# Kernel optimization log

Hardware: AMD Instinct MI355X
Metric: run time of the kernel (lower is better)

## Reference

```python
import jax, jax.numpy as jnp
import numpy as np

B, T, D = 2, 2048, 1024
H, HD = 16, 64
MAX_LEN = 2048


def setup_inputs() -> dict:
    key = jax.random.key(0)
    ks = jax.random.split(key, 7)
    s = 0.02
    return {
        "x": jax.random.normal(ks[0], (B, T, D), dtype=jnp.float32),
        "qkv_w": jax.random.normal(ks[1], (3 * D, D), dtype=jnp.float32) * s,
        "qkv_b": jax.random.normal(ks[2], (3 * D,), dtype=jnp.float32) * s,
        "out_w": jax.random.normal(ks[3], (D, D), dtype=jnp.float32) * s,
        "out_b": jax.random.normal(ks[4], (D,), dtype=jnp.float32) * s,
        "rel_pos": jax.random.normal(ks[5], (2 * MAX_LEN - 1, HD), dtype=jnp.float32),
        "rpe_w": jax.random.normal(ks[6], (HD,), dtype=jnp.float32) * s,
    }


def reference(x, qkv_w, qkv_b, out_w, out_b, rel_pos, rpe_w):
    Bq, Tq, Dq = x.shape
    scale = HD ** -0.5
    qkv = x @ qkv_w.T + qkv_b  # [B,T,3D]
    qkv = qkv.reshape(Bq, Tq, 3, H, HD)
    q = qkv[:, :, 0].transpose(0, 2, 1, 3)  # [B,H,T,HD]
    k = qkv[:, :, 1].transpose(0, 2, 1, 3)
    v = qkv[:, :, 2].transpose(0, 2, 1, 3)
    scores = jnp.einsum('bhqd,bhkd->bhqk', q, k) * scale  # [B,H,T,T]
    # relative position bias: gather rel embeddings, project to scalar
    rel_idx = jnp.arange(Tq)[None, :] - jnp.arange(Tq)[:, None] + MAX_LEN - 1  # [T,T]
    bias = (rel_pos @ rpe_w)[rel_idx]  # project first (cheap), then gather -> [T,T]
    scores = scores + bias[None, None]
    attn = jax.nn.softmax(scores, axis=-1)
    out = jnp.einsum('bhqk,bhkd->bhqd', attn, v)  # [B,H,T,HD]
    out = out.transpose(0, 2, 1, 3).reshape(Bq, Tq, Dq)
    return out @ out_w.T + out_b
```

## Files before the change

kernel.cpp:

```cpp
#include <hip/hip_runtime.h>
#include <math.h>

#define B_ 2
#define T_ 2048
#define D_ 1024
#define H_ 16
#define HD_ 64
#define MAXLEN_ 2048
#define N3D_ 3072
#define M_ (B_ * T_)
#define KA 1024

#define SCALE_L2E 0.18033688011116215f
#define L2E 1.4426950408889634f

typedef unsigned short ushort_t;
typedef __attribute__((ext_vector_type(8))) short short8;
typedef __attribute__((ext_vector_type(4))) float floatx4;
#define MFMA16(a, b, c) __builtin_amdgcn_mfma_f32_16x16x32_bf16(a, b, c, 0, 0, 0)

static __device__ __forceinline__ ushort_t f2bf(float f) {
    unsigned u = __float_as_uint(f);
    unsigned r = (u + 0x7FFFu + ((u >> 16) & 1u)) >> 16;
    return (ushort_t)r;
}
static __device__ __forceinline__ unsigned pack2bf(float a, float b) {
    unsigned ua = __float_as_uint(a), ub = __float_as_uint(b);
    ua = ua + 0x7FFFu + ((ua >> 16) & 1u);
    ub = ub + 0x7FFFu + ((ub >> 16) & 1u);
    return (ua >> 16) | (ub & 0xFFFF0000u);
}

static __device__ __forceinline__ void gld16(const ushort_t* g, ushort_t* l) {
    __builtin_amdgcn_global_load_lds(
        (const __attribute__((address_space(1))) void*)g,
        (__attribute__((address_space(3))) void*)l, 16, 0, 0);
}

__global__ __launch_bounds__(256) void cvt_all(
    const float* __restrict__ x, const float* __restrict__ qw,
    const float* __restrict__ ow,
    ushort_t* __restrict__ Xc, ushort_t* __restrict__ QWc,
    ushort_t* __restrict__ OWc)
{
    const int row = blockIdx.x;
    const float* src; ushort_t* dst; int r;
    if (row < M_)            { src = x;  dst = Xc;  r = row; }
    else if (row < M_ + N3D_){ src = qw; dst = QWc; r = row - M_; }
    else                     { src = ow; dst = OWc; r = row - M_ - N3D_; }
    const int c = threadIdx.x * 4;
    float4 v = *(const float4*)(src + (size_t)r * 1024 + c);
    ushort4 hv;
    hv.x = f2bf(v.x); hv.y = f2bf(v.y); hv.z = f2bf(v.z); hv.w = f2bf(v.w);
    *(ushort4*)(dst + (size_t)r * KA + c) = hv;
}

__global__ __launch_bounds__(256) void qkv_mfma(
    const ushort_t* __restrict__ Ac, const ushort_t* __restrict__ Bc,
    const float* __restrict__ bias,
    ushort_t* __restrict__ Qs, ushort_t* __restrict__ Khi,
    ushort_t* __restrict__ Vt)
{
    __shared__ __align__(16) ushort_t As[16 * 512];
    __shared__ __align__(16) ushort_t Bs[16 * 512];
    const int tid = threadIdx.x;
    const int wv = tid >> 6, lane = tid & 63;
    const int l16 = lane & 15, quad = lane >> 4;
    const int wm = wv & 1, wn = wv >> 1;
    const int m0 = blockIdx.y * 128, n0 = blockIdx.x * 128;

    floatx4 acc[4][4];
#pragma unroll
    for (int i = 0; i < 4; ++i)
#pragma unroll
        for (int j = 0; j < 4; ++j) acc[i][j] = (floatx4){0.f, 0.f, 0.f, 0.f};

    for (int k0 = 0; k0 < KA; k0 += 64) {
        __syncthreads();
#pragma unroll
        for (int c = 0; c < 4; ++c) {
            const int b = wv * 4 + c;
            const int i = b >> 1, ks = b & 1;
            const int k = k0 + ks * 32 + quad * 8;
            gld16(Ac + (size_t)(m0 + i * 16 + l16) * KA + k, As + b * 512);
            gld16(Bc + (size_t)(n0 + i * 16 + l16) * KA + k, Bs + b * 512);
        }
        __syncthreads();
#pragma unroll
        for (int ks = 0; ks < 2; ++ks) {
            short8 af[4], bf[4];
#pragma unroll
            for (int ii = 0; ii < 4; ++ii)
                af[ii] = *(const short8*)(As + ((wm * 4 + ii) * 2 + ks) * 512 + lane * 8);
#pragma unroll
            for (int jj = 0; jj < 4; ++jj)
                bf[jj] = *(const short8*)(Bs + ((wn * 4 + jj) * 2 + ks) * 512 + lane * 8);
#pragma unroll
            for (int ii = 0; ii < 4; ++ii)
#pragma unroll
                for (int jj = 0; jj < 4; ++jj)
                    acc[ii][jj] = MFMA16(af[ii], bf[jj], acc[ii][jj]);
        }
    }

#pragma unroll
    for (int ii = 0; ii < 4; ++ii) {
#pragma unroll
        for (int r = 0; r < 4; ++r) {
            const int m = m0 + wm * 64 + ii * 16 + quad * 4 + r;
            const int bb = m >> 11, t = m & 2047;
#pragma unroll
            for (int jj = 0; jj < 4; ++jj) {
                const int n = n0 + wn * 64 + jj * 16 + l16;
                const int c = n >> 10, h = (n >> 6) & 15, hd = n & 63;
                const float v = acc[ii][jj][r] + bias[n];
                const size_t idx = (((size_t)bb * H_ + h) * T_ + t) * HD_ + hd;
                if (c == 0) { Qs[idx] = f2bf(v * SCALE_L2E); }
                else if (c == 1) { Khi[idx] = f2bf(v); }
                else { Vt[(((size_t)bb * H_ + h) * HD_ + hd) * T_ + t] = f2bf(v); }
            }
        }
    }
}

__global__ __launch_bounds__(256) void out_mfma(
    const ushort_t* __restrict__ Ac, const ushort_t* __restrict__ Bc,
    const float* __restrict__ bias, float* __restrict__ Out)
{
    __shared__ __align__(16) ushort_t As[16 * 512];
    __shared__ __align__(16) ushort_t Bs[8 * 512];
    const int tid = threadIdx.x;
    const int wv = tid >> 6, lane = tid & 63;
    const int l16 = lane & 15, quad = lane >> 4;
    const int wm = wv & 1, wn = wv >> 1;
    const int m0 = blockIdx.y * 128, n0 = blockIdx.x * 64;

    floatx4 acc[4][2];
#pragma unroll
    for (int i = 0; i < 4; ++i)
#pragma unroll
        for (int j = 0; j < 2; ++j) acc[i][j] = (floatx4){0.f, 0.f, 0.f, 0.f};

    for (int k0 = 0; k0 < KA; k0 += 64) {
        __syncthreads();
#pragma unroll
        for (int c = 0; c < 4; ++c) {
            const int b = wv * 4 + c;
            const int i = b >> 1, ks = b & 1;
            const int k = k0 + ks * 32 + quad * 8;
            gld16(Ac + (size_t)(m0 + i * 16 + l16) * KA + k, As + b * 512);
        }
#pragma unroll
        for (int c = 0; c < 2; ++c) {
            const int b = wv * 2 + c;
            const int j = b >> 1, ks = b & 1;
            const int k = k0 + ks * 32 + quad * 8;
            gld16(Bc + (size_t)(n0 + j * 16 + l16) * KA + k, Bs + b * 512);
        }
        __syncthreads();
#pragma unroll
        for (int ks = 0; ks < 2; ++ks) {
            short8 af[4], bf[2];
#pragma unroll
            for (int ii = 0; ii < 4; ++ii)
                af[ii] = *(const short8*)(As + ((wm * 4 + ii) * 2 + ks) * 512 + lane * 8);
#pragma unroll
            for (int jj = 0; jj < 2; ++jj)
                bf[jj] = *(const short8*)(Bs + ((wn * 2 + jj) * 2 + ks) * 512 + lane * 8);
#pragma unroll
            for (int ii = 0; ii < 4; ++ii)
#pragma unroll
                for (int jj = 0; jj < 2; ++jj)
                    acc[ii][jj] = MFMA16(af[ii], bf[jj], acc[ii][jj]);
        }
    }

#pragma unroll
    for (int ii = 0; ii < 4; ++ii) {
#pragma unroll
        for (int r = 0; r < 4; ++r) {
            const int m = m0 + wm * 64 + ii * 16 + quad * 4 + r;
#pragma unroll
            for (int jj = 0; jj < 2; ++jj) {
                const int n = n0 + wn * 32 + jj * 16 + l16;
                Out[(size_t)m * D_ + n] = acc[ii][jj][r] + bias[n];
            }
        }
    }
}

__global__ __launch_bounds__(64) void rpe_project(
    const float* __restrict__ rel_pos, const float* __restrict__ rpe_w,
    float* __restrict__ biasp)
{
    const int i = blockIdx.x;
    const int lane = threadIdx.x;
    float v = rel_pos[(size_t)i * HD_ + lane] * rpe_w[lane];
#pragma unroll
    for (int off = 32; off; off >>= 1) v += __shfl_down(v, off);
    if (lane == 0) biasp[i] = v * L2E;
}

__global__ __launch_bounds__(256) void attn_mfma(
    const ushort_t* __restrict__ Qs, const ushort_t* __restrict__ Khi,
    const ushort_t* __restrict__ Vt, const float* __restrict__ biasp,
    ushort_t* __restrict__ AOc)
{
    __shared__ __align__(16) ushort_t KS[8 * 512];
    __shared__ __align__(16) ushort_t VS[8 * 512];
    __shared__ __align__(16) ushort_t PS[4][2 * 512];

    const int i = blockIdx.x;
    const int bh = (i & 7) + 8 * (i >> 8);
    const int q0 = ((i >> 3) & 31) * 64;
    const int tid = threadIdx.x;
    const int wv = tid >> 6, lane = tid & 63;
    const int l16 = lane & 15, quad = lane >> 4;

    const int q = q0 + wv * 16 + l16;
    const size_t qoff = ((size_t)bh * T_ + q) * HD_ + quad * 8;
    const short8 qh0 = *(const short8*)(Qs + qoff);
    const short8 qh1 = *(const short8*)(Qs + qoff + 32);

    float l_r = 0.f;
    floatx4 o_acc[4];
#pragma unroll
    for (int g2 = 0; g2 < 4; ++g2) o_acc[g2] = (floatx4){0.f, 0.f, 0.f, 0.f};

    const ushort_t* gK = Khi + (size_t)bh * T_ * HD_;
    const ushort_t* gV = Vt + (size_t)bh * HD_ * T_;
    const int biasbase = 2047 + quad * 4 - q;

    const int qdbase = quad >> 1;
    ushort_t* pw = PS[wv];

    for (int k0 = 0; k0 < T_; k0 += 64) {
        __syncthreads();
        {
            const size_t krow = (size_t)(k0 + wv * 16 + l16) * HD_ + quad * 8;
            gld16(gK + krow,      KS + (wv * 2 + 0) * 512);
            gld16(gK + krow + 32, KS + (wv * 2 + 1) * 512);
            const size_t vrow = (size_t)(wv * 16 + l16) * T_ + k0 + quad * 8;
            gld16(gV + vrow,      VS + (wv * 2 + 0) * 512);
            gld16(gV + vrow + 32, VS + (wv * 2 + 1) * 512);
        }
        float4 bb[4];
#pragma unroll
        for (int g = 0; g < 4; ++g)
            __builtin_memcpy(&bb[g], biasp + (biasbase + k0 + g * 16), 16);
        __syncthreads();

#pragma unroll
        for (int g = 0; g < 4; ++g) {
            const short8 kh0 = *(const short8*)(KS + (g * 2 + 0) * 512 + lane * 8);
            const short8 kh1 = *(const short8*)(KS + (g * 2 + 1) * 512 + lane * 8);
            floatx4 a = (floatx4){0.f, 0.f, 0.f, 0.f};
            a = MFMA16(kh0, qh0, a);
            a = MFMA16(kh1, qh1, a);
            const float* bp = (const float*)&bb[g];
            float p0 = __builtin_amdgcn_exp2f(a[0] + bp[0]);
            float p1 = __builtin_amdgcn_exp2f(a[1] + bp[1]);
            float p2 = __builtin_amdgcn_exp2f(a[2] + bp[2]);
            float p3 = __builtin_amdgcn_exp2f(a[3] + bp[3]);
            l_r += (p0 + p1) + (p2 + p3);
            uint2 pkd;
            pkd.x = pack2bf(p0, p1);
            pkd.y = pack2bf(p2, p3);
            const int qd = 2 * (g & 1) + qdbase;
            *(uint2*)(pw + (g >> 1) * 512 + (qd * 16 + l16) * 8 + (quad & 1) * 4) = pkd;
        }
        const short8 p0 = *(const short8*)(pw + lane * 8);
        const short8 p1 = *(const short8*)(pw + 512 + lane * 8);

#pragma unroll
        for (int g2 = 0; g2 < 4; ++g2) {
            const short8 v0 = *(const short8*)(VS + (g2 * 2 + 0) * 512 + lane * 8);
            const short8 v1 = *(const short8*)(VS + (g2 * 2 + 1) * 512 + lane * 8);
            o_acc[g2] = MFMA16(v0, p0, o_acc[g2]);
            o_acc[g2] = MFMA16(v1, p1, o_acc[g2]);
        }
    }

    l_r += __shfl_xor(l_r, 16);
    l_r += __shfl_xor(l_r, 32);
    const float inv = 1.0f / l_r;
    const int bb2 = bh >> 4, h2 = bh & 15;
    const size_t m = (size_t)bb2 * T_ + q;
#pragma unroll
    for (int g2 = 0; g2 < 4; ++g2) {
        ushort4 hv;
        hv.x = f2bf(o_acc[g2][0] * inv);
        hv.y = f2bf(o_acc[g2][1] * inv);
        hv.z = f2bf(o_acc[g2][2] * inv);
        hv.w = f2bf(o_acc[g2][3] * inv);
        *(ushort4*)(AOc + m * KA + h2 * 64 + g2 * 16 + quad * 4) = hv;
    }
}

extern "C" void kernel_launch(void* const* d_in, const int* in_sizes, int n_in,
                              void* d_out, int out_size, void* d_ws, size_t ws_size,
                              hipStream_t stream)
{
    const float* x       = (const float*)d_in[0];
    const float* qkv_w   = (const float*)d_in[1];
    const float* qkv_b   = (const float*)d_in[2];
    const float* out_w   = (const float*)d_in[3];
    const float* out_b   = (const float*)d_in[4];
    const float* rel_pos = (const float*)d_in[5];
    const float* rpe_w   = (const float*)d_in[6];
    float* out = (float*)d_out;

    const size_t QE = (size_t)B_ * H_ * T_ * HD_;
    ushort_t* Qs  = (ushort_t*)d_ws;
    ushort_t* Khi = Qs  + QE;
    ushort_t* Vt  = Khi + QE;
    ushort_t* Xc  = Vt  + QE;
    ushort_t* QWc = Xc  + (size_t)M_ * KA;
    ushort_t* OWc = QWc + (size_t)N3D_ * KA;
    ushort_t* AOc = OWc + (size_t)D_ * KA;
    float* biasp  = (float*)(AOc + (size_t)M_ * KA);

    cvt_all<<<M_ + N3D_ + D_, 256, 0, stream>>>(x, qkv_w, out_w, Xc, QWc, OWc);
    rpe_project<<<2 * MAXLEN_ - 1, 64, 0, stream>>>(rel_pos, rpe_w, biasp);

    qkv_mfma<<<dim3(N3D_ / 128, M_ / 128), 256, 0, stream>>>(
        Xc, QWc, qkv_b, Qs, Khi, Vt);
    attn_mfma<<<1024, 256, 0, stream>>>(Qs, Khi, Vt, biasp, AOc);
    out_mfma<<<dim3(D_ / 64, M_ / 128), 256, 0, stream>>>(
        AOc, OWc, out_b, out);
}
```

Baseline: 282.9 us.

## Restructure attention kernel to 32x32 MFMA tiles with register-resident K/V

Rewrites the attention kernel around 32x32x16 bf16 MFMAs. Each wave owns a 32-key by 32-query score tile and a 32-head-dim slice of the output. K and V fragments are loaded straight from global memory into registers and prefetched one tile ahead, so the K/V LDS staging is gone. P is exchanged between waves through a double-buffered, XOR-swizzled LDS buffer with a single barrier per tile, and the row sums are combined across waves at the end. The P conversion now uses truncation instead of round-to-nearest bf16, which is slightly less accurate, and K/V reuse now relies on caches rather than shared memory.

Measured after the change: 377.2 us. 33.3% more time.

```diff
diff --git a/kernel.cpp b/kernel.cpp
--- a/kernel.cpp
+++ b/kernel.cpp
@@ -17,7 +17,9 @@
 typedef unsigned short ushort_t;
 typedef __attribute__((ext_vector_type(8))) short short8;
 typedef __attribute__((ext_vector_type(4))) float floatx4;
+typedef __attribute__((ext_vector_type(16))) float floatx16;
 #define MFMA16(a, b, c) __builtin_amdgcn_mfma_f32_16x16x32_bf16(a, b, c, 0, 0, 0)
+#define MFMA32(a, b, c) __builtin_amdgcn_mfma_f32_32x32x16_bf16(a, b, c, 0, 0, 0)
 
 static __device__ __forceinline__ ushort_t f2bf(float f) {
     unsigned u = __float_as_uint(f);
@@ -29,6 +31,9 @@
     ua = ua + 0x7FFFu + ((ua >> 16) & 1u);
     ub = ub + 0x7FFFu + ((ub >> 16) & 1u);
     return (ua >> 16) | (ub & 0xFFFF0000u);
+}
+static __device__ __forceinline__ unsigned packrtz(float a, float b) {
+    return __builtin_amdgcn_perm(__float_as_uint(b), __float_as_uint(a), 0x07060302u);
 }
 
 static __device__ __forceinline__ void gld16(const ushort_t* g, ushort_t* l) {
@@ -206,94 +211,95 @@
     const ushort_t* __restrict__ Vt, const float* __restrict__ biasp,
     ushort_t* __restrict__ AOc)
 {
-    __shared__ __align__(16) ushort_t KS[8 * 512];
-    __shared__ __align__(16) ushort_t VS[8 * 512];
-    __shared__ __align__(16) ushort_t PS[4][2 * 512];
+    __shared__ __align__(16) ushort_t PS[2][4096];
+    __shared__ float LS[2][64];
 
     const int i = blockIdx.x;
     const int bh = (i & 7) + 8 * (i >> 8);
     const int q0 = ((i >> 3) & 31) * 64;
     const int tid = threadIdx.x;
     const int wv = tid >> 6, lane = tid & 63;
-    const int l16 = lane & 15, quad = lane >> 4;
-
-    const int q = q0 + wv * 16 + l16;
-    const size_t qoff = ((size_t)bh * T_ + q) * HD_ + quad * 8;
-    const short8 qh0 = *(const short8*)(Qs + qoff);
-    const short8 qh1 = *(const short8*)(Qs + qoff + 32);
-
-    float l_r = 0.f;
-    floatx4 o_acc[4];
-#pragma unroll
-    for (int g2 = 0; g2 < 4; ++g2) o_acc[g2] = (floatx4){0.f, 0.f, 0.f, 0.f};
-
-    const ushort_t* gK = Khi + (size_t)bh * T_ * HD_;
-    const ushort_t* gV = Vt + (size_t)bh * HD_ * T_;
-    const int biasbase = 2047 + quad * 4 - q;
-
-    const int qdbase = quad >> 1;
-    ushort_t* pw = PS[wv];
-
-    for (int k0 = 0; k0 < T_; k0 += 64) {
-        __syncthreads();
-        {
-            const size_t krow = (size_t)(k0 + wv * 16 + l16) * HD_ + quad * 8;
-            gld16(gK + krow,      KS + (wv * 2 + 0) * 512);
-            gld16(gK + krow + 32, KS + (wv * 2 + 1) * 512);
-            const size_t vrow = (size_t)(wv * 16 + l16) * T_ + k0 + quad * 8;
-            gld16(gV + vrow,      VS + (wv * 2 + 0) * 512);
-            gld16(gV + vrow + 32, VS + (wv * 2 + 1) * 512);
-        }
-        float4 bb[4];
-#pragma unroll
-        for (int g = 0; g < 4; ++g)
-            __builtin_memcpy(&bb[g], biasp + (biasbase + k0 + g * 16), 16);
-        __syncthreads();
-
-#pragma unroll
-        for (int g = 0; g < 4; ++g) {
-            const short8 kh0 = *(const short8*)(KS + (g * 2 + 0) * 512 + lane * 8);
-            const short8 kh1 = *(const short8*)(KS + (g * 2 + 1) * 512 + lane * 8);
-            floatx4 a = (floatx4){0.f, 0.f, 0.f, 0.f};
-            a = MFMA16(kh0, qh0, a);
-            a = MFMA16(kh1, qh1, a);
-            const float* bp = (const float*)&bb[g];
-            float p0 = __builtin_amdgcn_exp2f(a[0] + bp[0]);
-            float p1 = __builtin_amdgcn_exp2f(a[1] + bp[1]);
-            float p2 = __builtin_amdgcn_exp2f(a[2] + bp[2]);
-            float p3 = __builtin_amdgcn_exp2f(a[3] + bp[3]);
-            l_r += (p0 + p1) + (p2 + p3);
-            uint2 pkd;
-            pkd.x = pack2bf(p0, p1);
-            pkd.y = pack2bf(p2, p3);
-            const int qd = 2 * (g & 1) + qdbase;
-            *(uint2*)(pw + (g >> 1) * 512 + (qd * 16 + l16) * 8 + (quad & 1) * 4) = pkd;
-        }
-        const short8 p0 = *(const short8*)(pw + lane * 8);
-        const short8 p1 = *(const short8*)(pw + 512 + lane * 8);
-
-#pragma unroll
-        for (int g2 = 0; g2 < 4; ++g2) {
-            const short8 v0 = *(const short8*)(VS + (g2 * 2 + 0) * 512 + lane * 8);
-            const short8 v1 = *(const short8*)(VS + (g2 * 2 + 1) * 512 + lane * 8);
-            o_acc[g2] = MFMA16(v0, p0, o_acc[g2]);
-            o_acc[g2] = MFMA16(v1, p1, o_acc[g2]);
-        }
-    }
-
-    l_r += __shfl_xor(l_r, 16);
-    l_r += __shfl_xor(l_r, 32);
-    const float inv = 1.0f / l_r;
+    const int l32 = lane & 31, half = lane >> 5;
+    const int rw = wv & 1, cw = wv >> 1;
+
+    const int qcol = q0 + cw * 32 + l32;
+    const int qx = l32 & 7;
+
+    const ushort_t* gQ = Qs + ((size_t)bh * T_ + qcol) * HD_ + half * 8;
+    short8 qf[4];
+#pragma unroll
+    for (int m = 0; m < 4; ++m) qf[m] = *(const short8*)(gQ + 16 * m);
+
+    const ushort_t* gK = Khi + ((size_t)bh * T_ + rw * 32 + l32) * HD_ + half * 8;
+    const ushort_t* gV = Vt  + ((size_t)bh * HD_ + rw * 32 + l32) * T_ + half * 8;
+
+    short8 kf[4], vf[4];
+#pragma unroll
+    for (int m = 0; m < 4; ++m) {
+        kf[m] = *(const short8*)(gK + 16 * m);
+        vf[m] = *(const short8*)(gV + 16 * m);
+    }
+
+    floatx16 o_acc;
+#pragma unroll
+    for (int r = 0; r < 16; ++r) o_acc[r] = 0.f;
+    float l_part = 0.f;
+
+    const int ibias = 2047 + rw * 32 + half * 4 - qcol;
+
+    for (int t = 0; t < 32; ++t) {
+        const int k0 = t * 64;
+        floatx16 s;
+#pragma unroll
+        for (int r = 0; r < 16; ++r) s[r] = 0.f;
+#pragma unroll
+        for (int m = 0; m < 4; ++m) s = MFMA32(kf[m], qf[m], s);
+#pragma unroll
+        for (int m = 0; m < 4; ++m)
+            kf[m] = *(const short8*)(gK + (size_t)(k0 + 64) * HD_ + 16 * m);
+
+        ushort_t* pw = PS[t & 1] + (size_t)(cw * 32 + l32) * 64;
+#pragma unroll
+        for (int c = 0; c < 4; ++c) {
+            float4 bb;
+            __builtin_memcpy(&bb, biasp + (ibias + k0 + 8 * c), 16);
+            float p0 = __builtin_amdgcn_exp2f(s[4 * c + 0] + bb.x);
+            float p1 = __builtin_amdgcn_exp2f(s[4 * c + 1] + bb.y);
+            float p2 = __builtin_amdgcn_exp2f(s[4 * c + 2] + bb.z);
+            float p3 = __builtin_amdgcn_exp2f(s[4 * c + 3] + bb.w);
+            l_part += (p0 + p1) + (p2 + p3);
+            uint2 pk;
+            pk.x = packrtz(p0, p1);
+            pk.y = packrtz(p2, p3);
+            *(uint2*)(pw + (((c + 4 * rw) ^ qx) * 8 + half * 4)) = pk;
+        }
+        __syncthreads();
+
+        const ushort_t* pr = PS[t & 1] + (size_t)(cw * 32 + l32) * 64;
+#pragma unroll
+        for (int m = 0; m < 4; ++m) {
+            const short8 pf = *(const short8*)(pr + ((2 * m + half) ^ qx) * 8);
+            o_acc = MFMA32(vf[m], pf, o_acc);
+        }
+#pragma unroll
+        for (int m = 0; m < 4; ++m)
+            vf[m] = *(const short8*)(gV + (k0 + 64) + 16 * m);
+    }
+
+    l_part += __shfl_xor(l_part, 32);
+    if (half == 0) LS[rw][cw * 32 + l32] = l_part;
+    __syncthreads();
+    const float inv = 1.0f / (LS[0][cw * 32 + l32] + LS[1][cw * 32 + l32]);
+
     const int bb2 = bh >> 4, h2 = bh & 15;
-    const size_t m = (size_t)bb2 * T_ + q;
-#pragma unroll
-    for (int g2 = 0; g2 < 4; ++g2) {
-        ushort4 hv;
-        hv.x = f2bf(o_acc[g2][0] * inv);
-        hv.y = f2bf(o_acc[g2][1] * inv);
-        hv.z = f2bf(o_acc[g2][2] * inv);
-        hv.w = f2bf(o_acc[g2][3] * inv);
-        *(ushort4*)(AOc + m * KA + h2 * 64 + g2 * 16 + quad * 4) = hv;
+    const size_t mrow = (size_t)bb2 * T_ + qcol;
+#pragma unroll
+    for (int c = 0; c < 4; ++c) {
+        const int hd = rw * 32 + c * 8 + half * 4;
+        uint2 pk;
+        pk.x = pack2bf(o_acc[4 * c + 0] * inv, o_acc[4 * c + 1] * inv);
+        pk.y = pack2bf(o_acc[4 * c + 2] * inv, o_acc[4 * c + 3] * inv);
+        *(uint2*)(AOc + mrow * KA + h2 * 64 + hd) = pk;
     }
 }
 
```

## Split attention key range in two and add combine kernel

Applied to the files above, without the earlier changes.

The attention kernel now splits the key dimension into two halves, launching twice as many blocks. Each block writes unnormalized fp32 partial outputs and row sums. A new combine kernel adds the partials, normalizes, and writes bf16 into the layout the output projection expects. This raises parallelism and shortens per-block loops, but adds fp32 partial traffic and an extra launch.

Result: slower. 296.2 us (+4.7%).

```diff
diff --git a/kernel.cpp b/kernel.cpp
--- a/kernel.cpp
+++ b/kernel.cpp
@@ -10,6 +10,7 @@
 #define N3D_ 3072
 #define M_ (B_ * T_)
 #define KA 1024
+#define QE_ 4194304
 
 #define SCALE_L2E 0.18033688011116215f
 #define L2E 1.4426950408889634f
@@ -204,15 +205,19 @@
 __global__ __launch_bounds__(256) void attn_mfma(
     const ushort_t* __restrict__ Qs, const ushort_t* __restrict__ Khi,
     const ushort_t* __restrict__ Vt, const float* __restrict__ biasp,
-    ushort_t* __restrict__ AOc)
+    float* __restrict__ OP, float* __restrict__ LP)
 {
     __shared__ __align__(16) ushort_t KS[8 * 512];
     __shared__ __align__(16) ushort_t VS[8 * 512];
     __shared__ __align__(16) ushort_t PS[4][2 * 512];
 
     const int i = blockIdx.x;
-    const int bh = (i & 7) + 8 * (i >> 8);
-    const int q0 = ((i >> 3) & 31) * 64;
+    const int j = i >> 3;
+    const int q0 = (j & 31) * 64;
+    const int split = (j >> 5) & 1;
+    const int bh = (i & 7) + 8 * (j >> 6);
+    const int kbase = split * 1024;
+
     const int tid = threadIdx.x;
     const int wv = tid >> 6, lane = tid & 63;
     const int l16 = lane & 15, quad = lane >> 4;
@@ -234,7 +239,8 @@
     const int qdbase = quad >> 1;
     ushort_t* pw = PS[wv];
 
-    for (int k0 = 0; k0 < T_; k0 += 64) {
+    for (int t = 0; t < 16; ++t) {
+        const int k0 = kbase + t * 64;
         __syncthreads();
         {
             const size_t krow = (size_t)(k0 + wv * 16 + l16) * HD_ + quad * 8;
@@ -283,18 +289,36 @@
 
     l_r += __shfl_xor(l_r, 16);
     l_r += __shfl_xor(l_r, 32);
-    const float inv = 1.0f / l_r;
-    const int bb2 = bh >> 4, h2 = bh & 15;
-    const size_t m = (size_t)bb2 * T_ + q;
+    const size_t obase = (size_t)split * QE_ + ((size_t)bh * T_ + q) * HD_;
 #pragma unroll
     for (int g2 = 0; g2 < 4; ++g2) {
-        ushort4 hv;
-        hv.x = f2bf(o_acc[g2][0] * inv);
-        hv.y = f2bf(o_acc[g2][1] * inv);
-        hv.z = f2bf(o_acc[g2][2] * inv);
-        hv.w = f2bf(o_acc[g2][3] * inv);
-        *(ushort4*)(AOc + m * KA + h2 * 64 + g2 * 16 + quad * 4) = hv;
-    }
+        float4 v;
+        v.x = o_acc[g2][0]; v.y = o_acc[g2][1];
+        v.z = o_acc[g2][2]; v.w = o_acc[g2][3];
+        *(float4*)(OP + obase + g2 * 16 + quad * 4) = v;
+    }
+    if (quad == 0) LP[split * (B_ * H_ * T_) + bh * T_ + q] = l_r;
+}
+
+__global__ __launch_bounds__(256) void attn_combine(
+    const float* __restrict__ OP, const float* __restrict__ LP,
+    ushort_t* __restrict__ AOc)
+{
+    const int flat = blockIdx.x * 256 + threadIdx.x;
+    const int bh = flat >> 15;
+    const int rem = flat & 32767;
+    const int q = rem >> 4;
+    const int hd4 = (rem & 15) * 4;
+    const size_t base = ((size_t)bh * T_ + q) * HD_ + hd4;
+    float4 a = *(const float4*)(OP + base);
+    float4 b = *(const float4*)(OP + (size_t)QE_ + base);
+    const float l = LP[bh * T_ + q] + LP[B_ * H_ * T_ + bh * T_ + q];
+    const float inv = 1.0f / l;
+    uint2 pk;
+    pk.x = pack2bf((a.x + b.x) * inv, (a.y + b.y) * inv);
+    pk.y = pack2bf((a.z + b.z) * inv, (a.w + b.w) * inv);
+    const int bb = bh >> 4, h2 = bh & 15;
+    *(uint2*)(AOc + ((size_t)bb * T_ + q) * KA + h2 * 64 + hd4) = pk;
 }
 
 extern "C" void kernel_launch(void* const* d_in, const int* in_sizes, int n_in,
@@ -310,7 +334,7 @@
     const float* rpe_w   = (const float*)d_in[6];
     float* out = (float*)d_out;
 
-    const size_t QE = (size_t)B_ * H_ * T_ * HD_;
+    const size_t QE = QE_;
     ushort_t* Qs  = (ushort_t*)d_ws;
     ushort_t* Khi = Qs  + QE;
     ushort_t* Vt  = Khi + QE;
@@ -319,13 +343,16 @@
     ushort_t* OWc = QWc + (size_t)N3D_ * KA;
     ushort_t* AOc = OWc + (size_t)D_ * KA;
     float* biasp  = (float*)(AOc + (size_t)M_ * KA);
+    float* OP     = biasp + 4352;
+    float* LP     = OP + 2 * QE;
 
     cvt_all<<<M_ + N3D_ + D_, 256, 0, stream>>>(x, qkv_w, out_w, Xc, QWc, OWc);
     rpe_project<<<2 * MAXLEN_ - 1, 64, 0, stream>>>(rel_pos, rpe_w, biasp);
 
     qkv_mfma<<<dim3(N3D_ / 128, M_ / 128), 256, 0, stream>>>(
         Xc, QWc, qkv_b, Qs, Khi, Vt);
-    attn_mfma<<<1024, 256, 0, stream>>>(Qs, Khi, Vt, biasp, AOc);
+    attn_mfma<<<2048, 256, 0, stream>>>(Qs, Khi, Vt, biasp, OP, LP);
+    attn_combine<<<4096, 256, 0, stream>>>(OP, LP, AOc);
     out_mfma<<<dim3(D_ / 64, M_ / 128), 256, 0, stream>>>(
         AOc, OWc, out_b, out);
 }
```

## Double-buffer K/V tiles in LDS to overlap loads with attention compute

Applied to the files above, without the earlier changes.

The attention kernel now keeps two LDS buffers each for K and V. It prefetches the next 64-key tile into the spare buffer while the current tile feeds the QK and PV MFMAs, which cuts the two barriers per iteration down to one placed at the end of the loop. The aim is to hide global-to-LDS load latency behind compute. The cost is twice the K/V shared memory, which may lower occupancy. The output epilogue also switches to the packed bf16 conversion helper instead of four scalar conversions.

Result: no change. 278.0 us (-1.8%).

```diff
diff --git a/kernel.cpp b/kernel.cpp
--- a/kernel.cpp
+++ b/kernel.cpp
@@ -206,8 +206,8 @@
     const ushort_t* __restrict__ Vt, const float* __restrict__ biasp,
     ushort_t* __restrict__ AOc)
 {
-    __shared__ __align__(16) ushort_t KS[8 * 512];
-    __shared__ __align__(16) ushort_t VS[8 * 512];
+    __shared__ __align__(16) ushort_t KS[2][8 * 512];
+    __shared__ __align__(16) ushort_t VS[2][8 * 512];
     __shared__ __align__(16) ushort_t PS[4][2 * 512];
 
     const int i = blockIdx.x;
@@ -234,26 +234,36 @@
     const int qdbase = quad >> 1;
     ushort_t* pw = PS[wv];
 
-    for (int k0 = 0; k0 < T_; k0 += 64) {
-        __syncthreads();
-        {
-            const size_t krow = (size_t)(k0 + wv * 16 + l16) * HD_ + quad * 8;
-            gld16(gK + krow,      KS + (wv * 2 + 0) * 512);
-            gld16(gK + krow + 32, KS + (wv * 2 + 1) * 512);
-            const size_t vrow = (size_t)(wv * 16 + l16) * T_ + k0 + quad * 8;
-            gld16(gV + vrow,      VS + (wv * 2 + 0) * 512);
-            gld16(gV + vrow + 32, VS + (wv * 2 + 1) * 512);
+    const size_t kstage = (size_t)(wv * 16 + l16) * HD_ + quad * 8;
+    const size_t vstage = (size_t)(wv * 16 + l16) * T_ + quad * 8;
+
+    gld16(gK + kstage,              KS[0] + (wv * 2 + 0) * 512);
+    gld16(gK + kstage + 32,         KS[0] + (wv * 2 + 1) * 512);
+    gld16(gV + vstage,              VS[0] + (wv * 2 + 0) * 512);
+    gld16(gV + vstage + 32,         VS[0] + (wv * 2 + 1) * 512);
+    __syncthreads();
+
+    for (int t = 0; t < 32; ++t) {
+        const int k0 = t * 64;
+        const int buf = t & 1, nbuf = buf ^ 1;
+
+        if (t < 31) {
+            const size_t koff = kstage + (size_t)(k0 + 64) * HD_;
+            gld16(gK + koff,      KS[nbuf] + (wv * 2 + 0) * 512);
+            gld16(gK + koff + 32, KS[nbuf] + (wv * 2 + 1) * 512);
+            const size_t voff = vstage + (size_t)(k0 + 64);
+            gld16(gV + voff,      VS[nbuf] + (wv * 2 + 0) * 512);
+            gld16(gV + voff + 32, VS[nbuf] + (wv * 2 + 1) * 512);
         }
         float4 bb[4];
 #pragma unroll
         for (int g = 0; g < 4; ++g)
             __builtin_memcpy(&bb[g], biasp + (biasbase + k0 + g * 16), 16);
-        __syncthreads();
 
 #pragma unroll
         for (int g = 0; g < 4; ++g) {
-            const short8 kh0 = *(const short8*)(KS + (g * 2 + 0) * 512 + lane * 8);
-            const short8 kh1 = *(const short8*)(KS + (g * 2 + 1) * 512 + lane * 8);
+            const short8 kh0 = *(const short8*)(KS[buf] + (g * 2 + 0) * 512 + lane * 8);
+            const short8 kh1 = *(const short8*)(KS[buf] + (g * 2 + 1) * 512 + lane * 8);
             floatx4 a = (floatx4){0.f, 0.f, 0.f, 0.f};
             a = MFMA16(kh0, qh0, a);
             a = MFMA16(kh1, qh1, a);
@@ -274,11 +284,12 @@
 
 #pragma unroll
         for (int g2 = 0; g2 < 4; ++g2) {
-            const short8 v0 = *(const short8*)(VS + (g2 * 2 + 0) * 512 + lane * 8);
-            const short8 v1 = *(const short8*)(VS + (g2 * 2 + 1) * 512 + lane * 8);
+            const short8 v0 = *(const short8*)(VS[buf] + (g2 * 2 + 0) * 512 + lane * 8);
+            const short8 v1 = *(const short8*)(VS[buf] + (g2 * 2 + 1) * 512 + lane * 8);
             o_acc[g2] = MFMA16(v0, p0, o_acc[g2]);
             o_acc[g2] = MFMA16(v1, p1, o_acc[g2]);
         }
+        __syncthreads();
     }
 
     l_r += __shfl_xor(l_r, 16);
@@ -288,12 +299,10 @@
     const size_t m = (size_t)bb2 * T_ + q;
 #pragma unroll
     for (int g2 = 0; g2 < 4; ++g2) {
-        ushort4 hv;
-        hv.x = f2bf(o_acc[g2][0] * inv);
-        hv.y = f2bf(o_acc[g2][1] * inv);
-        hv.z = f2bf(o_acc[g2][2] * inv);
-        hv.w = f2bf(o_acc[g2][3] * inv);
-        *(ushort4*)(AOc + m * KA + h2 * 64 + g2 * 16 + quad * 4) = hv;
+        uint2 pk;
+        pk.x = pack2bf(o_acc[g2][0] * inv, o_acc[g2][1] * inv);
+        pk.y = pack2bf(o_acc[g2][2] * inv, o_acc[g2][3] * inv);
+        *(uint2*)(AOc + m * KA + h2 * 64 + g2 * 16 + quad * 4) = pk;
     }
 }
 
```
